# Kernel tuning notes

Hardware: AMD Instinct MI355X
Metric: run time of the kernel (lower is better)

Reference implementation:

```python
import jax, jax.numpy as jnp
import numpy as np

N_NODES = 50000
N_EDGES = 800000
IN_CH = 128
OUT_CH = 64
HEADS = 4
NEG_SLOPE = 0.2


def gat_layer(x, src, dst, W, a_src, a_dst, b, n):
    """One GATConv (PyG semantics, self-loops already in src/dst).
    x:[n,Fin], W:[Fin,H*C], a_src/a_dst:[H,C], b:[H*C]. Returns [n,H*C] (concat heads)."""
    H, C = a_src.shape
    h = (x @ W).reshape(n, H, C)                      # [n,H,C]
    alpha_s = jnp.einsum('nhc,hc->nh', h, a_src)      # [n,H]
    alpha_d = jnp.einsum('nhc,hc->nh', h, a_dst)
    e = jax.nn.leaky_relu(alpha_s[src] + alpha_d[dst], NEG_SLOPE)  # [E,H]
    m = jax.ops.segment_max(e, dst, num_segments=n)   # per-dst-node max (stable softmax)
    p = jnp.exp(e - m[dst])
    denom = jax.ops.segment_sum(p, dst, num_segments=n)
    alpha = p / (denom[dst] + 1e-16)                  # [E,H]
    out = jax.ops.segment_sum(h[src] * alpha[:, :, None], dst, num_segments=n)
    return out.reshape(n, H * C) + b


def setup_inputs() -> dict:
    key = jax.random.key(0)
    ks = jax.random.split(key, 10)
    x = jax.random.normal(ks[0], (N_NODES, IN_CH), dtype=jnp.float32)
    edge_index = jax.random.randint(ks[1], (2, N_EDGES), 0, N_NODES, dtype=jnp.int64)
    s = 0.05
    W1 = jax.random.normal(ks[2], (IN_CH, HEADS * OUT_CH), dtype=jnp.float32) * s
    a_src1 = jax.random.normal(ks[3], (HEADS, OUT_CH), dtype=jnp.float32) * s
    a_dst1 = jax.random.normal(ks[4], (HEADS, OUT_CH), dtype=jnp.float32) * s
    b1 = jnp.zeros((HEADS * OUT_CH,), dtype=jnp.float32)
    W2 = jax.random.normal(ks[5], (HEADS * OUT_CH, OUT_CH), dtype=jnp.float32) * s
    a_src2 = jax.random.normal(ks[6], (1, OUT_CH), dtype=jnp.float32) * s
    a_dst2 = jax.random.normal(ks[7], (1, OUT_CH), dtype=jnp.float32) * s
    b2 = jnp.zeros((OUT_CH,), dtype=jnp.float32)
    return {"x": x, "edge_index": edge_index, "W1": W1, "a_src1": a_src1,
            "a_dst1": a_dst1, "b1": b1, "W2": W2, "a_src2": a_src2,
            "a_dst2": a_dst2, "b2": b2}


def reference(x, edge_index, W1, a_src1, a_dst1, b1, W2, a_src2, a_dst2, b2):
    n = x.shape[0]
    # PyG GATConv adds self-loops by default
    loops = jnp.arange(n, dtype=edge_index.dtype)
    src = jnp.concatenate([edge_index[0], loops])
    dst = jnp.concatenate([edge_index[1], loops])
    h = jax.nn.relu(gat_layer(x, src, dst, W1, a_src1, a_dst1, b1, n))
    return gat_layer(h, src, dst, W2, a_src2, a_dst2, b2, n)
```

## Files before the change

kernel.cpp:

```cpp
#include <hip/hip_runtime.h>
#include <math.h>

#define N_NODES   50000
#define E0_EDGES  800000
#define E_TOT     (E0_EDGES + N_NODES)
#define FIN       128
#define F1        256
#define H1        4
#define C2        64
#define NEG_SLOPE 0.2f

typedef short bf16x8 __attribute__((ext_vector_type(8)));
typedef float f32x4  __attribute__((ext_vector_type(4)));

__device__ __forceinline__ unsigned short f2bf(float f) {
  unsigned u = __float_as_uint(f);
  u = (u + 0x7FFFu + ((u >> 16) & 1u)) >> 16;
  return (unsigned short)u;
}
__device__ __forceinline__ float bf2f(unsigned short h) {
  return __uint_as_float((unsigned)h << 16);
}
__device__ __forceinline__ float leaky(float v) {
  return v >= 0.f ? v : NEG_SLOPE * v;
}

__global__ __launch_bounds__(256) void deg_kernel(
    const int* __restrict__ ei, int* __restrict__ count) {
  int e = blockIdx.x * 256 + threadIdx.x;
  if (e >= E_TOT) return;
  int dst = (e < E0_EDGES) ? ei[E0_EDGES + e] : (e - E0_EDGES);
  atomicAdd(&count[dst], 1);
}

__global__ __launch_bounds__(256) void scanA_kernel(
    const int* __restrict__ cnt, int* __restrict__ bsum, int n) {
  int i = blockIdx.x * 256 + threadIdx.x;
  int v = (i < n) ? cnt[i] : 0;
#pragma unroll
  for (int d = 1; d < 64; d <<= 1) v += __shfl_xor(v, d);
  __shared__ int ws[4];
  if ((threadIdx.x & 63) == 0) ws[threadIdx.x >> 6] = v;
  __syncthreads();
  if (threadIdx.x == 0) bsum[blockIdx.x] = ws[0] + ws[1] + ws[2] + ws[3];
}

__global__ __launch_bounds__(256) void scanB_kernel(
    const int* __restrict__ bsum, int* __restrict__ bexcl,
    int* __restrict__ off_n, int nb) {
  const int t = threadIdx.x, lane = t & 63, wid = t >> 6;
  int v = (t < nb) ? bsum[t] : 0;
  int sv = v;
#pragma unroll
  for (int d = 1; d < 64; d <<= 1) {
    int u = __shfl_up(sv, d);
    if (lane >= d) sv += u;
  }
  __shared__ int ws[4];
  if (lane == 63) ws[wid] = sv;
  __syncthreads();
  int add = 0;
  for (int k = 0; k < wid; ++k) add += ws[k];
  int incl = sv + add;
  if (t < nb) bexcl[t] = incl - v;
  if (t == 255) off_n[0] = incl;
}

__global__ __launch_bounds__(256) void scanC_kernel(
    const int* __restrict__ cnt, const int* __restrict__ bexcl,
    int* __restrict__ off, int n) {
  const int t = threadIdx.x, lane = t & 63, wid = t >> 6;
  int i = blockIdx.x * 256 + t;
  int v = (i < n) ? cnt[i] : 0;
  int sv = v;
#pragma unroll
  for (int d = 1; d < 64; d <<= 1) {
    int u = __shfl_up(sv, d);
    if (lane >= d) sv += u;
  }
  __shared__ int ws[4];
  if (lane == 63) ws[wid] = sv;
  __syncthreads();
  int add = 0;
  for (int k = 0; k < wid; ++k) add += ws[k];
  if (i < n) off[i] = sv + add - v + bexcl[blockIdx.x];
}

__global__ __launch_bounds__(256) void scatter_kernel(
    const int* __restrict__ ei, const int* __restrict__ offset,
    int* __restrict__ cursor, int* __restrict__ csr_src) {
  int e = blockIdx.x * 256 + threadIdx.x;
  if (e >= E_TOT) return;
  int src, dst;
  if (e < E0_EDGES) { src = ei[e]; dst = ei[E0_EDGES + e]; }
  else              { src = e - E0_EDGES; dst = src; }
  int pos = offset[dst] + atomicAdd(&cursor[dst], 1);
  csr_src[pos] = src;
}

__global__ __launch_bounds__(256) void gemm1_kernel(
    const float* __restrict__ A, const float* __restrict__ B,
    unsigned short* __restrict__ C, float* __restrict__ as1,
    float* __restrict__ ad1, const float* __restrict__ a_s,
    const float* __restrict__ a_d, int M) {
  constexpr int K = FIN, BN = 128, KP = K + 8, NF = BN / 16;
  __shared__ unsigned short BT[BN * KP];
  const int tid = threadIdx.x, lane = tid & 63, wid = tid >> 6;
  const int gy = blockIdx.y, n0 = gy * BN;

  for (int idx = tid; idx < K * (BN / 8); idx += 256) {
    int k = idx >> 4;
    int c = idx & 15;
    const float* src = &B[(size_t)k * F1 + n0 + c * 8];
    float4 lo = *reinterpret_cast<const float4*>(src);
    float4 hi = *reinterpret_cast<const float4*>(src + 4);
    int nb = c * 8;
    BT[(nb + 0) * KP + k] = f2bf(lo.x); BT[(nb + 1) * KP + k] = f2bf(lo.y);
    BT[(nb + 2) * KP + k] = f2bf(lo.z); BT[(nb + 3) * KP + k] = f2bf(lo.w);
    BT[(nb + 4) * KP + k] = f2bf(hi.x); BT[(nb + 5) * KP + k] = f2bf(hi.y);
    BT[(nb + 6) * KP + k] = f2bf(hi.z); BT[(nb + 7) * KP + k] = f2bf(hi.w);
  }
  __syncthreads();

  const int r0 = (blockIdx.x * 4 + wid) * 16;
  if (r0 >= M) return;
  const int nlane = lane & 15;
  const int kg    = (lane >> 4) * 8;
  const int arow  = min(r0 + nlane, M - 1);

  f32x4 acc[NF];
#pragma unroll
  for (int nf = 0; nf < NF; ++nf) acc[nf] = (f32x4){0.f, 0.f, 0.f, 0.f};

  const float* ap = &A[(size_t)arow * K + kg];
#pragma unroll
  for (int kk = 0; kk < K; kk += 32) {
    float4 v0 = *reinterpret_cast<const float4*>(ap + kk);
    float4 v1 = *reinterpret_cast<const float4*>(ap + kk + 4);
    bf16x8 a;
    a[0] = (short)f2bf(v0.x); a[1] = (short)f2bf(v0.y);
    a[2] = (short)f2bf(v0.z); a[3] = (short)f2bf(v0.w);
    a[4] = (short)f2bf(v1.x); a[5] = (short)f2bf(v1.y);
    a[6] = (short)f2bf(v1.z); a[7] = (short)f2bf(v1.w);
#pragma unroll
    for (int nf = 0; nf < NF; ++nf) {
      bf16x8 b = *reinterpret_cast<const bf16x8*>(&BT[(nf * 16 + nlane) * KP + kk + kg]);
      acc[nf] = __builtin_amdgcn_mfma_f32_16x16x32_bf16(a, b, acc[nf], 0, 0, 0);
    }
  }

  const int crow = r0 + (lane >> 4) * 4;
#pragma unroll
  for (int nf = 0; nf < NF; ++nf) {
    const int cc = n0 + nf * 16 + nlane;
#pragma unroll
    for (int j = 0; j < 4; ++j) {
      int rr = crow + j;
      if (rr < M) C[(size_t)rr * F1 + cc] = f2bf(acc[nf][j]);
    }
  }

#pragma unroll
  for (int j = 0; j < 4; ++j) {
    float ps0 = 0.f, ps1 = 0.f, pd0 = 0.f, pd1 = 0.f;
#pragma unroll
    for (int nf = 0; nf < NF; ++nf) {
      int col = n0 + nf * 16 + nlane;
      float v = acc[nf][j];
      float sc = a_s[col], dc = a_d[col];
      if (nf < 4) { ps0 = fmaf(v, sc, ps0); pd0 = fmaf(v, dc, pd0); }
      else        { ps1 = fmaf(v, sc, ps1); pd1 = fmaf(v, dc, pd1); }
    }
#pragma unroll
    for (int d = 1; d < 16; d <<= 1) {
      ps0 += __shfl_xor(ps0, d); ps1 += __shfl_xor(ps1, d);
      pd0 += __shfl_xor(pd0, d); pd1 += __shfl_xor(pd1, d);
    }
    int row = crow + j;
    if (nlane == 0 && row < M) {
      float2 s2 = {ps0, ps1}, d2 = {pd0, pd1};
      *reinterpret_cast<float2*>(&as1[row * 4 + gy * 2]) = s2;
      *reinterpret_cast<float2*>(&ad1[row * 4 + gy * 2]) = d2;
    }
  }
}

__global__ __launch_bounds__(256) void gemm2_kernel(
    const unsigned short* __restrict__ A, const float* __restrict__ B,
    unsigned short* __restrict__ C, float* __restrict__ as2,
    float* __restrict__ ad2, const float* __restrict__ a_s,
    const float* __restrict__ a_d, int M) {
  constexpr int K = F1, BN = 64, KP = K + 8, NF = BN / 16;
  __shared__ unsigned short BT[BN * KP];
  const int tid = threadIdx.x, lane = tid & 63, wid = tid >> 6;

  for (int idx = tid; idx < K * (BN / 8); idx += 256) {
    int k = idx >> 3;
    int c = idx & 7;
    const float* src = &B[(size_t)k * C2 + c * 8];
    float4 lo = *reinterpret_cast<const float4*>(src);
    float4 hi = *reinterpret_cast<const float4*>(src + 4);
    int nb = c * 8;
    BT[(nb + 0) * KP + k] = f2bf(lo.x); BT[(nb + 1) * KP + k] = f2bf(lo.y);
    BT[(nb + 2) * KP + k] = f2bf(lo.z); BT[(nb + 3) * KP + k] = f2bf(lo.w);
    BT[(nb + 4) * KP + k] = f2bf(hi.x); BT[(nb + 5) * KP + k] = f2bf(hi.y);
    BT[(nb + 6) * KP + k] = f2bf(hi.z); BT[(nb + 7) * KP + k] = f2bf(hi.w);
  }
  __syncthreads();

  const int r0 = (blockIdx.x * 4 + wid) * 16;
  if (r0 >= M) return;
  const int nlane = lane & 15;
  const int kg    = (lane >> 4) * 8;
  const int arow  = min(r0 + nlane, M - 1);

  f32x4 acc[NF];
#pragma unroll
  for (int nf = 0; nf < NF; ++nf) acc[nf] = (f32x4){0.f, 0.f, 0.f, 0.f};

  const unsigned short* ap = &A[(size_t)arow * K + kg];
#pragma unroll
  for (int kk = 0; kk < K; kk += 32) {
    bf16x8 a = *reinterpret_cast<const bf16x8*>(ap + kk);
#pragma unroll
    for (int nf = 0; nf < NF; ++nf) {
      bf16x8 b = *reinterpret_cast<const bf16x8*>(&BT[(nf * 16 + nlane) * KP + kk + kg]);
      acc[nf] = __builtin_amdgcn_mfma_f32_16x16x32_bf16(a, b, acc[nf], 0, 0, 0);
    }
  }

  const int crow = r0 + (lane >> 4) * 4;
#pragma unroll
  for (int nf = 0; nf < NF; ++nf) {
    const int cc = nf * 16 + nlane;
#pragma unroll
    for (int j = 0; j < 4; ++j) {
      int rr = crow + j;
      if (rr < M) C[(size_t)rr * C2 + cc] = f2bf(acc[nf][j]);
    }
  }

#pragma unroll
  for (int j = 0; j < 4; ++j) {
    float ps = 0.f, pd = 0.f;
#pragma unroll
    for (int nf = 0; nf < NF; ++nf) {
      int col = nf * 16 + nlane;
      float v = acc[nf][j];
      ps = fmaf(v, a_s[col], ps);
      pd = fmaf(v, a_d[col], pd);
    }
#pragma unroll
    for (int d = 1; d < 16; d <<= 1) {
      ps += __shfl_xor(ps, d);
      pd += __shfl_xor(pd, d);
    }
    int row = crow + j;
    if (nlane == 0 && row < M) { as2[row] = ps; ad2[row] = pd; }
  }
}

__global__ __launch_bounds__(256) void aggregate1_kernel(
    const unsigned short* __restrict__ h1b, const float* __restrict__ as,
    const float* __restrict__ ad, const int* __restrict__ csr_src,
    const int* __restrict__ offset, const float* __restrict__ b1,
    unsigned short* __restrict__ out1b, int n) {
  const int lane = threadIdx.x & 63;
  const int node = blockIdx.x * 4 + (threadIdx.x >> 6);
  if (node >= n) return;
  const int beg = offset[node], end = offset[node + 1];
  const int hl = lane >> 4;
  const float4 advv = *reinterpret_cast<const float4*>(&ad[node * H1]);
  const float adv[4] = {advv.x, advv.y, advv.z, advv.w};

  float den[4] = {0.f, 0.f, 0.f, 0.f};
  for (int e = beg + lane; e < end; e += 64) {
    int s = csr_src[e];
    const float4 sv = *reinterpret_cast<const float4*>(&as[s * H1]);
    den[0] += __expf(leaky(sv.x + adv[0]));
    den[1] += __expf(leaky(sv.y + adv[1]));
    den[2] += __expf(leaky(sv.z + adv[2]));
    den[3] += __expf(leaky(sv.w + adv[3]));
  }
#pragma unroll
  for (int h = 0; h < 4; ++h) {
#pragma unroll
    for (int d = 1; d < 64; d <<= 1) den[h] += __shfl_xor(den[h], d);
    den[h] = 1.f / (den[h] + 1e-16f);
  }

  float4 acc = make_float4(0.f, 0.f, 0.f, 0.f);
  const float dh = den[hl], adh = adv[hl];
  const unsigned loff = (unsigned)(lane * 4);
  int e = beg;
  for (; e + 7 < end; e += 8) {
    int s[8];
    ushort4 r[8];
    float a[8];
#pragma unroll
    for (int i = 0; i < 8; ++i) s[i] = csr_src[e + i];
#pragma unroll
    for (int i = 0; i < 8; ++i)
      r[i] = *reinterpret_cast<const ushort4*>(h1b + (unsigned)(s[i] * F1) + loff);
#pragma unroll
    for (int i = 0; i < 8; ++i) a[i] = as[s[i] * H1 + hl];
#pragma unroll
    for (int i = 0; i < 8; ++i) {
      const float w = __expf(leaky(a[i] + adh)) * dh;
      acc.x = fmaf(w, bf2f(r[i].x), acc.x);
      acc.y = fmaf(w, bf2f(r[i].y), acc.y);
      acc.z = fmaf(w, bf2f(r[i].z), acc.z);
      acc.w = fmaf(w, bf2f(r[i].w), acc.w);
    }
  }
  for (; e < end; ++e) {
    const int s0 = csr_src[e];
    const float w = __expf(leaky(as[s0 * H1 + hl] + adh)) * dh;
    const ushort4 r0 = *reinterpret_cast<const ushort4*>(h1b + (unsigned)(s0 * F1) + loff);
    acc.x = fmaf(w, bf2f(r0.x), acc.x);
    acc.y = fmaf(w, bf2f(r0.y), acc.y);
    acc.z = fmaf(w, bf2f(r0.z), acc.z);
    acc.w = fmaf(w, bf2f(r0.w), acc.w);
  }
  const float4 bb = *reinterpret_cast<const float4*>(&b1[lane * 4]);
  ushort4 ob;
  ob.x = f2bf(fmaxf(acc.x + bb.x, 0.f));
  ob.y = f2bf(fmaxf(acc.y + bb.y, 0.f));
  ob.z = f2bf(fmaxf(acc.z + bb.z, 0.f));
  ob.w = f2bf(fmaxf(acc.w + bb.w, 0.f));
  *reinterpret_cast<ushort4*>(&out1b[(size_t)node * F1 + lane * 4]) = ob;
}

__global__ __launch_bounds__(256) void aggregate2_kernel(
    const unsigned short* __restrict__ h2b, const float* __restrict__ as,
    const float* __restrict__ ad, const int* __restrict__ csr_src,
    const int* __restrict__ offset, const float* __restrict__ b2,
    float* __restrict__ out, int n) {
  const int lane = threadIdx.x & 63;
  const int node = blockIdx.x * 4 + (threadIdx.x >> 6);
  if (node >= n) return;
  const int beg = offset[node], end = offset[node + 1];
  const float adv = ad[node];

  float den = 0.f;
  for (int e = beg + lane; e < end; e += 64)
    den += __expf(leaky(as[csr_src[e]] + adv));
#pragma unroll
  for (int d = 1; d < 64; d <<= 1) den += __shfl_xor(den, d);
  const float inv = 1.f / (den + 1e-16f);

  float acc = 0.f;
  int e = beg;
  for (; e + 7 < end; e += 8) {
    int s[8];
    unsigned short r[8];
    float a[8];
#pragma unroll
    for (int i = 0; i < 8; ++i) s[i] = csr_src[e + i];
#pragma unroll
    for (int i = 0; i < 8; ++i) r[i] = h2b[(unsigned)(s[i] * C2) + lane];
#pragma unroll
    for (int i = 0; i < 8; ++i) a[i] = as[s[i]];
#pragma unroll
    for (int i = 0; i < 8; ++i)
      acc = fmaf(__expf(leaky(a[i] + adv)) * inv, bf2f(r[i]), acc);
  }
  for (; e < end; ++e) {
    const int s0 = csr_src[e];
    acc = fmaf(__expf(leaky(as[s0] + adv)) * inv,
               bf2f(h2b[(unsigned)(s0 * C2) + lane]), acc);
  }
  out[(size_t)node * C2 + lane] = acc + b2[lane];
}

extern "C" void kernel_launch(void* const* d_in, const int* in_sizes, int n_in,
                              void* d_out, int out_size, void* d_ws, size_t ws_size,
                              hipStream_t stream) {
  const float* x      = (const float*)d_in[0];
  const int*   ei     = (const int*)d_in[1];
  const float* W1     = (const float*)d_in[2];
  const float* a_src1 = (const float*)d_in[3];
  const float* a_dst1 = (const float*)d_in[4];
  const float* b1     = (const float*)d_in[5];
  const float* W2     = (const float*)d_in[6];
  const float* a_src2 = (const float*)d_in[7];
  const float* a_dst2 = (const float*)d_in[8];
  const float* b2     = (const float*)d_in[9];
  float*       out    = (float*)d_out;

  const int n = N_NODES;
  const int nchunks = (n + 255) / 256;

  char* w = (char*)d_ws;
  unsigned short* h1b   = (unsigned short*)w; w += (size_t)n * F1 * 2;
  unsigned short* out1b = (unsigned short*)w; w += (size_t)n * F1 * 2;
  float*          as1   = (float*)w;          w += (size_t)n * H1 * 4;
  float*          ad1   = (float*)w;          w += (size_t)n * H1 * 4;
  float*          as2   = (float*)w;          w += 200192;
  float*          ad2   = (float*)w;          w += 200192;
  int*            cnt   = (int*)w;            w += 200192;
  int*            off   = (int*)w;            w += 200704;
  int*            cur   = (int*)w;            w += 200192;
  int*            bsum  = (int*)w;            w += 1024;
  int*            bexcl = (int*)w;            w += 1024;
  int*            csr   = (int*)w;            w += 3400192;
  unsigned short* h2b   = h1b;

  hipMemsetAsync(cnt, 0, (size_t)n * 4, stream);
  hipMemsetAsync(cur, 0, (size_t)n * 4, stream);
  deg_kernel<<<(E_TOT + 255) / 256, 256, 0, stream>>>(ei, cnt);
  scanA_kernel<<<nchunks, 256, 0, stream>>>(cnt, bsum, n);
  scanB_kernel<<<1, 256, 0, stream>>>(bsum, bexcl, &off[n], nchunks);
  scanC_kernel<<<nchunks, 256, 0, stream>>>(cnt, bexcl, off, n);
  scatter_kernel<<<(E_TOT + 255) / 256, 256, 0, stream>>>(ei, off, cur, csr);

  {
    dim3 grid((n + 63) / 64, 2);
    gemm1_kernel<<<grid, 256, 0, stream>>>(x, W1, h1b, as1, ad1, a_src1, a_dst1, n);
  }
  aggregate1_kernel<<<(n + 3) / 4, 256, 0, stream>>>(h1b, as1, ad1, csr, off, b1, out1b, n);

  {
    dim3 grid((n + 63) / 64, 1);
    gemm2_kernel<<<grid, 256, 0, stream>>>(out1b, W2, h2b, as2, ad2, a_src2, a_dst2, n);
  }
  aggregate2_kernel<<<(n + 3) / 4, 256, 0, stream>>>(h2b, as2, ad2, csr, off, b2, out, n);
}
```

Before: 339.4 us.

## Fuse softmax denominator into aggregation loop and merge workspace memsets

Both aggregation kernels drop their separate first pass over each node's edges that computed the softmax denominator. The unnormalized exp weights are now summed alongside the weighted feature accumulation, and the result is divided once at the end. This removes a second round of gathers of csr_src and attention scores plus the wavefront shuffle reductions. The cnt and cur buffers are also placed next to each other so one memset clears both. The trade-off is that no per-node max is subtracted, and exp overflow would only be avoided by keeping scores small.

```diff
diff --git a/kernel.cpp b/kernel.cpp
--- a/kernel.cpp
+++ b/kernel.cpp
@@ -270,28 +270,11 @@
   if (node >= n) return;
   const int beg = offset[node], end = offset[node + 1];
   const int hl = lane >> 4;
-  const float4 advv = *reinterpret_cast<const float4*>(&ad[node * H1]);
-  const float adv[4] = {advv.x, advv.y, advv.z, advv.w};
-
-  float den[4] = {0.f, 0.f, 0.f, 0.f};
-  for (int e = beg + lane; e < end; e += 64) {
-    int s = csr_src[e];
-    const float4 sv = *reinterpret_cast<const float4*>(&as[s * H1]);
-    den[0] += __expf(leaky(sv.x + adv[0]));
-    den[1] += __expf(leaky(sv.y + adv[1]));
-    den[2] += __expf(leaky(sv.z + adv[2]));
-    den[3] += __expf(leaky(sv.w + adv[3]));
-  }
-#pragma unroll
-  for (int h = 0; h < 4; ++h) {
-#pragma unroll
-    for (int d = 1; d < 64; d <<= 1) den[h] += __shfl_xor(den[h], d);
-    den[h] = 1.f / (den[h] + 1e-16f);
-  }
+  const float adh = ad[node * H1 + hl];
+  const unsigned loff = (unsigned)(lane * 4);
 
   float4 acc = make_float4(0.f, 0.f, 0.f, 0.f);
-  const float dh = den[hl], adh = adv[hl];
-  const unsigned loff = (unsigned)(lane * 4);
+  float den = 0.f;
   int e = beg;
   for (; e + 7 < end; e += 8) {
     int s[8];
@@ -306,7 +289,8 @@
     for (int i = 0; i < 8; ++i) a[i] = as[s[i] * H1 + hl];
 #pragma unroll
     for (int i = 0; i < 8; ++i) {
-      const float w = __expf(leaky(a[i] + adh)) * dh;
+      const float w = __expf(leaky(a[i] + adh));
+      den += w;
       acc.x = fmaf(w, bf2f(r[i].x), acc.x);
       acc.y = fmaf(w, bf2f(r[i].y), acc.y);
       acc.z = fmaf(w, bf2f(r[i].z), acc.z);
@@ -315,19 +299,21 @@
   }
   for (; e < end; ++e) {
     const int s0 = csr_src[e];
-    const float w = __expf(leaky(as[s0 * H1 + hl] + adh)) * dh;
+    const float w = __expf(leaky(as[s0 * H1 + hl] + adh));
+    den += w;
     const ushort4 r0 = *reinterpret_cast<const ushort4*>(h1b + (unsigned)(s0 * F1) + loff);
     acc.x = fmaf(w, bf2f(r0.x), acc.x);
     acc.y = fmaf(w, bf2f(r0.y), acc.y);
     acc.z = fmaf(w, bf2f(r0.z), acc.z);
     acc.w = fmaf(w, bf2f(r0.w), acc.w);
   }
+  const float inv = 1.f / (den + 1e-16f);
   const float4 bb = *reinterpret_cast<const float4*>(&b1[lane * 4]);
   ushort4 ob;
-  ob.x = f2bf(fmaxf(acc.x + bb.x, 0.f));
-  ob.y = f2bf(fmaxf(acc.y + bb.y, 0.f));
-  ob.z = f2bf(fmaxf(acc.z + bb.z, 0.f));
-  ob.w = f2bf(fmaxf(acc.w + bb.w, 0.f));
+  ob.x = f2bf(fmaxf(fmaf(acc.x, inv, bb.x), 0.f));
+  ob.y = f2bf(fmaxf(fmaf(acc.y, inv, bb.y), 0.f));
+  ob.z = f2bf(fmaxf(fmaf(acc.z, inv, bb.z), 0.f));
+  ob.w = f2bf(fmaxf(fmaf(acc.w, inv, bb.w), 0.f));
   *reinterpret_cast<ushort4*>(&out1b[(size_t)node * F1 + lane * 4]) = ob;
 }
 
@@ -342,14 +328,8 @@
   const int beg = offset[node], end = offset[node + 1];
   const float adv = ad[node];
 
+  float acc = 0.f;
   float den = 0.f;
-  for (int e = beg + lane; e < end; e += 64)
-    den += __expf(leaky(as[csr_src[e]] + adv));
-#pragma unroll
-  for (int d = 1; d < 64; d <<= 1) den += __shfl_xor(den, d);
-  const float inv = 1.f / (den + 1e-16f);
-
-  float acc = 0.f;
   int e = beg;
   for (; e + 7 < end; e += 8) {
     int s[8];
@@ -362,15 +342,19 @@
 #pragma unroll
     for (int i = 0; i < 8; ++i) a[i] = as[s[i]];
 #pragma unroll
-    for (int i = 0; i < 8; ++i)
-      acc = fmaf(__expf(leaky(a[i] + adv)) * inv, bf2f(r[i]), acc);
+    for (int i = 0; i < 8; ++i) {
+      const float w = __expf(leaky(a[i] + adv));
+      den += w;
+      acc = fmaf(w, bf2f(r[i]), acc);
+    }
   }
   for (; e < end; ++e) {
     const int s0 = csr_src[e];
-    acc = fmaf(__expf(leaky(as[s0] + adv)) * inv,
-               bf2f(h2b[(unsigned)(s0 * C2) + lane]), acc);
-  }
-  out[(size_t)node * C2 + lane] = acc + b2[lane];
+    const float w = __expf(leaky(as[s0] + adv));
+    den += w;
+    acc = fmaf(w, bf2f(h2b[(unsigned)(s0 * C2) + lane]), acc);
+  }
+  out[(size_t)node * C2 + lane] = fmaf(acc, 1.f / (den + 1e-16f), b2[lane]);
 }
 
 extern "C" void kernel_launch(void* const* d_in, const int* in_sizes, int n_in,
@@ -399,15 +383,14 @@
   float*          as2   = (float*)w;          w += 200192;
   float*          ad2   = (float*)w;          w += 200192;
   int*            cnt   = (int*)w;            w += 200192;
+  int*            cur   = (int*)w;            w += 200192;
   int*            off   = (int*)w;            w += 200704;
-  int*            cur   = (int*)w;            w += 200192;
   int*            bsum  = (int*)w;            w += 1024;
   int*            bexcl = (int*)w;            w += 1024;
   int*            csr   = (int*)w;            w += 3400192;
   unsigned short* h2b   = h1b;
 
-  hipMemsetAsync(cnt, 0, (size_t)n * 4, stream);
-  hipMemsetAsync(cur, 0, (size_t)n * 4, stream);
+  hipMemsetAsync(cnt, 0, 2 * 200192, stream);
   deg_kernel<<<(E_TOT + 255) / 256, 256, 0, stream>>>(ei, cnt);
   scanA_kernel<<<nchunks, 256, 0, stream>>>(cnt, bsum, n);
   scanB_kernel<<<1, 256, 0, stream>>>(bsum, bexcl, &off[n], nchunks);
```

Result: faster. 328.9 us (-3.1%).
